# Optimization experiments

Measured on AMD Instinct MI355X. Metric: run time of the kernel, lower is better.

## Reference

```python
import jax, jax.numpy as jnp
import numpy as np
import math

C = 512
NUM_HEADS = 4
GROUPS = 32  # group_count(512, 32)
EPS = 1e-5


def group_norm(x, gamma, beta):
    # x: [b, c, h, w]; normalize over (c//GROUPS, h, w) per group
    b, c, h, w = x.shape
    xg = x.reshape(b, GROUPS, -1)
    mu = jnp.mean(xg, axis=-1, keepdims=True)
    var = jnp.var(xg, axis=-1, keepdims=True)
    xn = ((xg - mu) * jax.lax.rsqrt(var + EPS)).reshape(b, c, h, w)
    return xn * gamma[None, :, None, None] + beta[None, :, None, None]


def setup_inputs() -> dict:
    key = jax.random.key(0)
    ks = jax.random.split(key, 5)
    b, h, w = 2, 64, 64
    x = jax.random.normal(ks[0], (b, C, h, w), dtype=jnp.float32)
    gn_w = jnp.ones((C,), dtype=jnp.float32)
    gn_b = jnp.zeros((C,), dtype=jnp.float32)
    s_qkv = 1.0 / math.sqrt(C)
    w_qkv = jax.random.uniform(ks[1], (3 * C, C), jnp.float32, -s_qkv, s_qkv)
    b_qkv = jax.random.uniform(ks[2], (3 * C,), jnp.float32, -s_qkv, s_qkv)
    w_proj = jax.random.uniform(ks[3], (C, C), jnp.float32, -s_qkv, s_qkv)
    b_proj = jax.random.uniform(ks[4], (C,), jnp.float32, -s_qkv, s_qkv)
    return {"x": x, "gn_w": gn_w, "gn_b": gn_b, "w_qkv": w_qkv,
            "b_qkv": b_qkv, "w_proj": w_proj, "b_proj": b_proj}


def reference(x, gn_w, gn_b, w_qkv, b_qkv, w_proj, b_proj):
    b, c, h, w = x.shape
    L = h * w
    nh = NUM_HEADS
    hd = c // nh
    residual = x
    xn = group_norm(x, gn_w, gn_b).reshape(b, c, L)
    # Conv1d with kernel_size=1 == channelwise linear: [b, 3c, L]
    qkv = jnp.einsum('bcl,oc->bol', xn, w_qkv) + b_qkv[None, :, None]
    q, k, v = jnp.split(qkv, 3, axis=1)
    q = q.reshape(b, nh, hd, L)
    k = k.reshape(b, nh, hd, L)
    v = v.reshape(b, nh, hd, L)
    scores = jnp.einsum('bncd,bnce->bnde', q, k) / math.sqrt(hd)
    attn = jax.nn.softmax(scores, axis=-1)
    out = jnp.einsum('bnde,bnce->bncd', attn, v).reshape(b, c, L)
    out = jnp.einsum('bcl,oc->bol', out, w_proj) + b_proj[None, :, None]
    return out.reshape(b, c, h, w) + residual
```

## Files before the change

### kernel.cpp

```cpp
#include <hip/hip_runtime.h>
#include <math.h>

typedef __bf16 bf16;
typedef __bf16 bf16x8 __attribute__((ext_vector_type(8)));
typedef __bf16 bf16x4 __attribute__((ext_vector_type(4)));
typedef float f32x4 __attribute__((ext_vector_type(4)));

#define QSCALE (0.08838834764831845f * 1.4426950408889634f)

__device__ __forceinline__ void gll16(const bf16* g, bf16* l) {
    __builtin_amdgcn_global_load_lds((const __attribute__((address_space(1))) void*)g,
                                     (__attribute__((address_space(3))) void*)l, 16, 0, 0);
}

__global__ void k_pre(const float* __restrict__ wqkv, const float* __restrict__ wproj,
                      const float* __restrict__ x,
                      bf16* __restrict__ wqkv_b, bf16* __restrict__ wproj_b,
                      float* __restrict__ part) {
    int blk = blockIdx.x;
    if (blk < 1024) {
        int i = blk * 256 + threadIdx.x;
        const int n1 = (1536 * 512) / 4;
        float4 v;
        bf16* dst;
        if (i < n1) { v = ((const float4*)wqkv)[i];      dst = wqkv_b + (size_t)i * 4; }
        else        { v = ((const float4*)wproj)[i - n1]; dst = wproj_b + (size_t)(i - n1) * 4; }
        bf16x4 o;
        o[0] = (bf16)v.x; o[1] = (bf16)v.y; o[2] = (bf16)v.z; o[3] = (bf16)v.w;
        *(bf16x4*)dst = o;
        return;
    }
    int b2 = blk - 1024;
    int grp = b2 >> 2, p = b2 & 3;
    const float4* src = (const float4*)(x + (size_t)grp * 65536 + (size_t)p * 16384);
    float s = 0.f, ss = 0.f;
    for (int it = 0; it < 16; ++it) {
        float4 v = src[threadIdx.x + it * 256];
        s  += v.x + v.y + v.z + v.w;
        ss += v.x * v.x + v.y * v.y + v.z * v.z + v.w * v.w;
    }
    for (int off = 32; off; off >>= 1) { s += __shfl_down(s, off); ss += __shfl_down(ss, off); }
    __shared__ float rs[4], rss[4];
    int wave = threadIdx.x >> 6;
    if ((threadIdx.x & 63) == 0) { rs[wave] = s; rss[wave] = ss; }
    __syncthreads();
    if (threadIdx.x == 0) {
        part[(grp * 4 + p) * 2]     = rs[0] + rs[1] + rs[2] + rs[3];
        part[(grp * 4 + p) * 2 + 1] = rss[0] + rss[1] + rss[2] + rss[3];
    }
}

__global__ __launch_bounds__(256) void k_gn_norm_t(const float* __restrict__ x, const float* __restrict__ gw,
                                                   const float* __restrict__ gb, const float* __restrict__ part,
                                                   bf16* __restrict__ xn_t) {
    __shared__ float sX[64 * 69];
    __shared__ float sMean[4], sRstd[4];
    int b = blockIdx.z, c0 = blockIdx.y * 64, l0 = blockIdx.x * 64;
    int t = threadIdx.x;
    if (t < 4) {
        int g = b * 32 + (c0 >> 4) + t;
        float S = 0.f, SS = 0.f;
        for (int p = 0; p < 4; ++p) { S += part[(g * 4 + p) * 2]; SS += part[(g * 4 + p) * 2 + 1]; }
        float mean = S * (1.f / 65536.f);
        float var  = SS * (1.f / 65536.f) - mean * mean;
        sMean[t] = mean;
        sRstd[t] = rsqrtf(var + 1e-5f);
    }
    __syncthreads();
    int cr = t >> 4, lq = t & 15;
    const float* xp = x + ((size_t)(b * 512 + c0)) * 4096 + l0;
    for (int i = 0; i < 4; ++i) {
        int c = cr + i * 16;
        int cg = c0 + c;
        float mean = sMean[c >> 4], rstd = sRstd[c >> 4];
        float ga = gw[cg] * rstd;
        float be = gb[cg] - mean * ga;
        float4 v = *(const float4*)(xp + (size_t)c * 4096 + lq * 4);
        float* d = &sX[c * 69 + lq * 4];
        d[0] = v.x * ga + be; d[1] = v.y * ga + be; d[2] = v.z * ga + be; d[3] = v.w * ga + be;
    }
    __syncthreads();
    int lr = t >> 3, cp = t & 7;
    bf16* dst = xn_t + ((size_t)b * 4096 + l0) * 512 + c0;
    for (int i = 0; i < 2; ++i) {
        int l = lr + i * 32;
        bf16x8 o;
        for (int j = 0; j < 8; ++j) o[j] = (bf16)sX[(cp * 8 + j) * 69 + l];
        *(bf16x8*)(dst + (size_t)l * 512 + cp * 8) = o;
    }
}

__global__ __launch_bounds__(256, 3) void k_gemm_qkv(
    const bf16* __restrict__ A, const bf16* __restrict__ W, const float* __restrict__ bias,
    bf16* __restrict__ qkT, bf16* __restrict__ vb) {
    constexpr int BUF = (128 + 128) * 32;
    __shared__ bf16 smem[17408];
    int bz = blockIdx.z;
    int m0 = blockIdx.y * 128, n0 = blockIdx.x * 128;
    int tid = threadIdx.x, lane = tid & 63, wave = tid >> 6;
    int lo = lane & 15, quad = lane >> 4;
    int mw = (wave >> 1) * 64, nw = (wave & 1) * 64;
    int srcswz = (((lane & 3) ^ ((lane >> 2) & 3) ^ ((lane >> 4) & 3)) * 8);
    const bf16* aptr[2]; int adst[2];
    const bf16* bptr[2]; int bdst[2];
    for (int i = 0; i < 2; ++i) {
        int r0 = wave * 32 + i * 16;
        int row = r0 + (lane >> 2);
        aptr[i] = A + (size_t)bz * (4096 * 512) + (size_t)(m0 + row) * 512 + srcswz;
        adst[i] = r0 * 32;
        bptr[i] = W + (size_t)(n0 + row) * 512 + srcswz;
        bdst[i] = 128 * 32 + r0 * 32;
    }
    f32x4 acc[4][4] = {};
    for (int i = 0; i < 2; ++i) {
        gll16(aptr[i], &smem[adst[i]]); aptr[i] += 32;
        gll16(bptr[i], &smem[bdst[i]]); bptr[i] += 32;
    }
    int sw = (quad ^ (lo & 3) ^ (lo >> 2)) * 8;
    for (int step = 0; step < 16; ++step) {
        int cur = step & 1;
        __syncthreads();
        if (step < 15) {
            bf16* nb = &smem[(cur ^ 1) * BUF];
            for (int i = 0; i < 2; ++i) {
                gll16(aptr[i], nb + adst[i]); aptr[i] += 32;
                gll16(bptr[i], nb + bdst[i]); bptr[i] += 32;
            }
        }
        const bf16* sA = &smem[cur * BUF];
        const bf16* sB = sA + 128 * 32;
        bf16x8 af[4], bfr[4];
        for (int t = 0; t < 4; ++t) af[t]  = *(const bf16x8*)&sA[(mw + t * 16 + lo) * 32 + sw];
        for (int t = 0; t < 4; ++t) bfr[t] = *(const bf16x8*)&sB[(nw + t * 16 + lo) * 32 + sw];
        for (int mt = 0; mt < 4; ++mt)
            for (int nt = 0; nt < 4; ++nt)
                acc[mt][nt] = __builtin_amdgcn_mfma_f32_16x16x32_bf16(af[mt], bfr[nt], acc[mt][nt], 0, 0, 0);
    }
    __syncthreads();
    bf16* sT = smem;
    bool isv = (n0 >= 1024);
    float sc = (n0 < 512) ? QSCALE : 1.f;
    for (int mt = 0; mt < 4; ++mt)
        for (int nt = 0; nt < 4; ++nt) {
            int c = nw + nt * 16 + lo;
            float bv = bias[n0 + c];
            for (int r = 0; r < 4; ++r) {
                int l = mw + mt * 16 + quad * 4 + r;
                float v = (acc[mt][nt][r] + bv) * sc;
                if (isv) sT[c * 136 + l] = (bf16)v;
                else     sT[l * 136 + c] = (bf16)v;
            }
        }
    __syncthreads();
    int row = tid >> 1, hh = tid & 1;
    if (isv) {
        bf16* dst = vb + (size_t)bz * (512 * 4096) + (size_t)(n0 - 1024 + row) * 4096 + m0;
        for (int j = 0; j < 8; ++j) {
            int ch = hh + j * 2;
            *(bf16x8*)(dst + ch * 8) = *(const bf16x8*)&sT[row * 136 + ch * 8];
        }
    } else {
        bf16* dst = qkT + (size_t)bz * (4096 * 1024) + (size_t)(m0 + row) * 1024 + n0;
        for (int j = 0; j < 8; ++j) {
            int ch = hh + j * 2;
            *(bf16x8*)(dst + ch * 8) = *(const bf16x8*)&sT[row * 136 + ch * 8];
        }
    }
}

__global__ __launch_bounds__(256, 3) void k_gemm_proj(
    const bf16* __restrict__ W, const bf16* __restrict__ Bm,
    const float* __restrict__ bias_m,
    float* __restrict__ outf, const float* __restrict__ resid) {
    constexpr int BUF = (64 + 128) * 64;
    __shared__ bf16 smem[2 * BUF];
    int bz = blockIdx.z;
    int m0 = blockIdx.y * 64, n0 = blockIdx.x * 128;
    int tid = threadIdx.x, lane = tid & 63, wave = tid >> 6;
    int lo = lane & 15, quad = lane >> 4;
    int lr = lane >> 3, ls = lane & 7;
    int mw = (wave >> 1) * 32, nw = (wave & 1) * 64;
    const bf16* aptr[2]; int adst[2];
    for (int i = 0; i < 2; ++i) {
        int r0 = wave * 16 + i * 8;
        int row = r0 + lr;
        aptr[i] = W + (size_t)(m0 + row) * 512 + ((ls ^ (row & 7)) * 8);
        adst[i] = r0 * 64;
    }
    const bf16* bptr[4]; int bdst[4];
    for (int i = 0; i < 4; ++i) {
        int r0 = wave * 32 + i * 8;
        int row = r0 + lr;
        bptr[i] = Bm + (size_t)bz * (4096 * 512) + (size_t)(n0 + row) * 512 + ((ls ^ (row & 7)) * 8);
        bdst[i] = 64 * 64 + r0 * 64;
    }
    f32x4 acc[2][4] = {};
    for (int i = 0; i < 2; ++i) { gll16(aptr[i], &smem[adst[i]]); aptr[i] += 64; }
    for (int i = 0; i < 4; ++i) { gll16(bptr[i], &smem[bdst[i]]); bptr[i] += 64; }
    for (int step = 0; step < 8; ++step) {
        int cur = step & 1;
        __syncthreads();
        if (step < 7) {
            bf16* nb = &smem[(cur ^ 1) * BUF];
            for (int i = 0; i < 2; ++i) { gll16(aptr[i], nb + adst[i]); aptr[i] += 64; }
            for (int i = 0; i < 4; ++i) { gll16(bptr[i], nb + bdst[i]); bptr[i] += 64; }
        }
        const bf16* sA = &smem[cur * BUF];
        const bf16* sB = sA + 64 * 64;
        for (int kk = 0; kk < 2; ++kk) {
            bf16x8 af[2], bfr[4];
            int sw = ((kk * 4 + quad) ^ (lo & 7)) * 8;
            for (int t = 0; t < 2; ++t) af[t]  = *(const bf16x8*)&sA[(mw + t * 16 + lo) * 64 + sw];
            for (int t = 0; t < 4; ++t) bfr[t] = *(const bf16x8*)&sB[(nw + t * 16 + lo) * 64 + sw];
            for (int mt = 0; mt < 2; ++mt)
                for (int nt = 0; nt < 4; ++nt)
                    acc[mt][nt] = __builtin_amdgcn_mfma_f32_16x16x32_bf16(af[mt], bfr[nt], acc[mt][nt], 0, 0, 0);
        }
    }
    for (int mt = 0; mt < 2; ++mt) {
        int rowb = m0 + mw + mt * 16 + quad * 4;
        for (int nt = 0; nt < 4; ++nt) {
            int col = n0 + nw + nt * 16 + lo;
            for (int r = 0; r < 4; ++r) {
                int row = rowb + r;
                size_t idx = (size_t)bz * (512 * 4096) + (size_t)row * 4096 + col;
                outf[idx] = acc[mt][nt][r] + bias_m[row] + resid[idx];
            }
        }
    }
}

__global__ __launch_bounds__(512, 2) void k_attn(const bf16* __restrict__ qkT, const bf16* __restrict__ vmat,
                                                 bf16* __restrict__ attnT) {
    __shared__ __align__(16) char smem[104448];
    bf16* sE = (bf16*)smem;
    float* sStat = (float*)(smem + 102400);
    int bidx = blockIdx.x;
    int bh = bidx & 7;
    int bb = bh >> 2, h = bh & 3;
    int l0 = (bidx >> 3) * 128;
    int tid = threadIdx.x, lane = tid & 63, wave = tid >> 6;
    int lo = lane & 15, quad = lane >> 4;
    int a = wave & 3, b2 = wave >> 2;
    int lr16 = lane >> 4, ls16 = lane & 15;
    int lr8 = lane >> 3, ls8 = lane & 7;
    const bf16* qbase = qkT + ((size_t)bb * 4096 + l0) * 1024 + h * 128;
    const bf16* kbase = qkT + (size_t)bb * 4096 * 1024 + 512 + h * 128;
    const bf16* vbase = vmat + (size_t)(bb * 512 + h * 128) * 4096;
    for (int i = 0; i < 4; ++i) {
        int r0 = wave * 16 + i * 4;
        int row = r0 + lr16;
        gll16(qbase + (size_t)row * 1024 + ((ls16 ^ (row & 15)) * 8), sE + r0 * 128);
    }
    __syncthreads();
    bf16x8 qf[2][4];
    for (int nt = 0; nt < 2; ++nt) {
        int row = a * 32 + nt * 16 + lo;
        for (int kk = 0; kk < 4; ++kk)
            qf[nt][kk] = *(const bf16x8*)&sE[row * 128 + (((kk * 4 + quad) ^ lo) * 8)];
    }
    __syncthreads();
    const bf16* kptr[2]; int kdst[2];
    const bf16* vptr[2]; int vdst[2];
    for (int i = 0; i < 2; ++i) {
        int r0 = wave * 8 + i * 4;
        int row = r0 + lr16;
        kptr[i] = kbase + (size_t)row * 1024 + ((ls16 ^ (row & 15)) * 8);
        kdst[i] = r0 * 128;
        int s0 = wave * 16 + i * 8;
        int srow = s0 + lr8;
        vptr[i] = vbase + (size_t)srow * 4096 + ((ls8 ^ (srow & 7)) * 8);
        vdst[i] = s0 * 64;
    }
    bf16* sPe = (bf16*)(smem + 65536) + wave * 1280;
    float l_r[2];
    l_r[0] = l_r[1] = 0.f;
    f32x4 oacc[8][2] = {};
    for (int i = 0; i < 2; ++i) { gll16(kptr[i], sE + kdst[i]); kptr[i] += (size_t)64 * 1024; }
    for (int i = 0; i < 2; ++i) { gll16(vptr[i], sE + 16384 + vdst[i]); vptr[i] += 64; }
    for (int it = 0; it < 64; ++it) {
        int cur = it & 1;
        __syncthreads();
        if (it < 63) {
            bf16* nk = sE + (cur ^ 1) * 8192;
            bf16* nv = sE + 16384 + (cur ^ 1) * 8192;
            for (int i = 0; i < 2; ++i) { gll16(kptr[i], nk + kdst[i]); kptr[i] += (size_t)64 * 1024; }
            for (int i = 0; i < 2; ++i) { gll16(vptr[i], nv + vdst[i]); vptr[i] += 64; }
        }
        const bf16* sK = sE + cur * 8192;
        const bf16* sV = sE + 16384 + cur * 8192;
        f32x4 s[2][2];
        for (int mt = 0; mt < 2; ++mt) {
            int krow = b2 * 32 + mt * 16 + lo;
            bf16x8 kf[4];
            for (int kk = 0; kk < 4; ++kk)
                kf[kk] = *(const bf16x8*)&sK[krow * 128 + (((kk * 4 + quad) ^ lo) * 8)];
            for (int nt = 0; nt < 2; ++nt) {
                f32x4 acc = {};
                for (int kk = 0; kk < 4; ++kk)
                    acc = __builtin_amdgcn_mfma_f32_16x16x32_bf16(kf[kk], qf[nt][kk], acc, 0, 0, 0);
                s[mt][nt] = acc;
            }
        }
        for (int nt = 0; nt < 2; ++nt) {
            float sm = 0.f;
            for (int mt = 0; mt < 2; ++mt) {
                bf16x4 pk;
                for (int r = 0; r < 4; ++r) {
                    float pv = __builtin_amdgcn_exp2f(s[mt][nt][r]);
                    sm += pv;
                    pk[r] = (bf16)pv;
                }
                *(bf16x4*)&sPe[(nt * 16 + lo) * 40 + mt * 16 + quad * 4] = pk;
            }
            l_r[nt] += sm;
        }
        bf16x8 pf[2];
        for (int nt = 0; nt < 2; ++nt)
            pf[nt] = *(const bf16x8*)&sPe[(nt * 16 + lo) * 40 + quad * 8];
        for (int mt2 = 0; mt2 < 8; ++mt2) {
            bf16x8 vf = *(const bf16x8*)&sV[(mt2 * 16 + lo) * 64 + (((b2 * 4 + quad) ^ (lo & 7)) * 8)];
            for (int nt = 0; nt < 2; ++nt)
                oacc[mt2][nt] = __builtin_amdgcn_mfma_f32_16x16x32_bf16(vf, pf[nt], oacc[mt2][nt], 0, 0, 0);
        }
    }
    for (int nt = 0; nt < 2; ++nt) {
        l_r[nt] += __shfl_xor(l_r[nt], 16);
        l_r[nt] += __shfl_xor(l_r[nt], 32);
    }
    __syncthreads();
    if (quad == 0) {
        for (int nt = 0; nt < 2; ++nt) {
            int qb = a * 32 + nt * 16 + lo;
            sStat[qb * 2 + b2] = l_r[nt];
        }
    }
    __syncthreads();
    float inv[2];
    for (int nt = 0; nt < 2; ++nt) {
        int qb = a * 32 + nt * 16 + lo;
        inv[nt] = 1.f / (sStat[qb * 2] + sStat[qb * 2 + 1]);
    }
    float* sOm = (float*)smem;
    bf16* sOut = (bf16*)(smem + 67584);
    if (b2 == 1) {
        for (int mt2 = 0; mt2 < 8; ++mt2)
            for (int nt = 0; nt < 2; ++nt)
                for (int r = 0; r < 4; ++r) {
                    int vc = mt2 * 16 + quad * 4 + r;
                    sOm[a * 4224 + vc * 33 + nt * 16 + lo] = oacc[mt2][nt][r];
                }
    }
    __syncthreads();
    if (b2 == 0) {
        for (int mt2 = 0; mt2 < 8; ++mt2)
            for (int nt = 0; nt < 2; ++nt)
                for (int r = 0; r < 4; ++r) {
                    int vc = mt2 * 16 + quad * 4 + r;
                    float v = (oacc[mt2][nt][r] + sOm[a * 4224 + vc * 33 + nt * 16 + lo]) * inv[nt];
                    sOut[(a * 32 + nt * 16 + lo) * 136 + vc] = (bf16)v;
                }
    }
    __syncthreads();
    bf16* dst = attnT + ((size_t)bb * 4096 + l0) * 512 + h * 128;
    for (int i = 0; i < 4; ++i) {
        int row = (tid >> 4) + i * 32;
        int chunk = tid & 15;
        bf16x8 v = *(const bf16x8*)&sOut[row * 136 + chunk * 8];
        *(bf16x8*)(dst + (size_t)row * 512 + chunk * 8) = v;
    }
}

extern "C" void kernel_launch(void* const* d_in, const int* in_sizes, int n_in,
                              void* d_out, int out_size, void* d_ws, size_t ws_size,
                              hipStream_t stream) {
    const float* x      = (const float*)d_in[0];
    const float* gn_w   = (const float*)d_in[1];
    const float* gn_b   = (const float*)d_in[2];
    const float* w_qkv  = (const float*)d_in[3];
    const float* b_qkv  = (const float*)d_in[4];
    const float* w_proj = (const float*)d_in[5];
    const float* b_proj = (const float*)d_in[6];
    float* out = (float*)d_out;
    char* ws = (char*)d_ws;
    bf16* wqkv_b  = (bf16*)(ws + 0);
    bf16* wproj_b = (bf16*)(ws + 1572864);
    bf16* xn_t    = (bf16*)(ws + 2097152);
    bf16* qkT     = (bf16*)(ws + 10485760);
    bf16* vb      = (bf16*)(ws + 27262976);
    bf16* attnT   = (bf16*)(ws + 35651584);
    float* part   = (float*)(ws + 44040192);

    k_pre<<<1280, 256, 0, stream>>>(w_qkv, w_proj, x, wqkv_b, wproj_b, part);
    k_gn_norm_t<<<dim3(64, 8, 2), 256, 0, stream>>>(x, gn_w, gn_b, part, xn_t);
    k_gemm_qkv<<<dim3(12, 32, 2), 256, 0, stream>>>(xn_t, wqkv_b, b_qkv, qkT, vb);
    k_attn<<<256, 512, 0, stream>>>(qkT, vb, attnT);
    k_gemm_proj<<<dim3(32, 8, 2), 256, 0, stream>>>(wproj_b, attnT, b_proj, out, x);
}
```

Before: 192.1 us.

## Single-buffer QKV GEMM with BK=64, XOR swizzle and block remapping

The QKV GEMM mainloop drops double-buffered BK=32 staging in favour of single-buffered BK=64 tiles. This halves the number of barrier-separated steps but removes the overlap between loads and MFMA. The LDS swizzle becomes an 8-way XOR over 64-element rows to avoid bank conflicts. Block indices are remapped so that consecutive workgroups spread across the tile space, aiming at better L2 locality across XCDs.

```diff
diff --git a/kernel.cpp b/kernel.cpp
--- a/kernel.cpp
+++ b/kernel.cpp
@@ -93,48 +93,45 @@
 __global__ __launch_bounds__(256, 3) void k_gemm_qkv(
     const bf16* __restrict__ A, const bf16* __restrict__ W, const float* __restrict__ bias,
     bf16* __restrict__ qkT, bf16* __restrict__ vb) {
-    constexpr int BUF = (128 + 128) * 32;
     __shared__ bf16 smem[17408];
-    int bz = blockIdx.z;
-    int m0 = blockIdx.y * 128, n0 = blockIdx.x * 128;
+    int linear = blockIdx.x + 12 * blockIdx.y + 384 * blockIdx.z;
+    int swz = (linear & 7) * 96 + (linear >> 3);
+    int n0 = (swz % 12) * 128;
+    int m0 = ((swz / 12) % 32) * 128;
+    int bz = swz / 384;
     int tid = threadIdx.x, lane = tid & 63, wave = tid >> 6;
     int lo = lane & 15, quad = lane >> 4;
+    int lr = lane >> 3, ls = lane & 7;
     int mw = (wave >> 1) * 64, nw = (wave & 1) * 64;
-    int srcswz = (((lane & 3) ^ ((lane >> 2) & 3) ^ ((lane >> 4) & 3)) * 8);
-    const bf16* aptr[2]; int adst[2];
-    const bf16* bptr[2]; int bdst[2];
-    for (int i = 0; i < 2; ++i) {
-        int r0 = wave * 32 + i * 16;
-        int row = r0 + (lane >> 2);
-        aptr[i] = A + (size_t)bz * (4096 * 512) + (size_t)(m0 + row) * 512 + srcswz;
-        adst[i] = r0 * 32;
-        bptr[i] = W + (size_t)(n0 + row) * 512 + srcswz;
-        bdst[i] = 128 * 32 + r0 * 32;
+    const bf16* aptr[4]; int adst[4];
+    const bf16* bptr[4]; int bdst[4];
+    for (int i = 0; i < 4; ++i) {
+        int r0 = wave * 32 + i * 8;
+        int row = r0 + lr;
+        aptr[i] = A + (size_t)bz * (4096 * 512) + (size_t)(m0 + row) * 512 + ((ls ^ (row & 7)) * 8);
+        adst[i] = r0 * 64;
+        bptr[i] = W + (size_t)(n0 + row) * 512 + ((ls ^ (row & 7)) * 8);
+        bdst[i] = 8192 + r0 * 64;
     }
     f32x4 acc[4][4] = {};
-    for (int i = 0; i < 2; ++i) {
-        gll16(aptr[i], &smem[adst[i]]); aptr[i] += 32;
-        gll16(bptr[i], &smem[bdst[i]]); bptr[i] += 32;
-    }
-    int sw = (quad ^ (lo & 3) ^ (lo >> 2)) * 8;
-    for (int step = 0; step < 16; ++step) {
-        int cur = step & 1;
+    for (int step = 0; step < 8; ++step) {
         __syncthreads();
-        if (step < 15) {
-            bf16* nb = &smem[(cur ^ 1) * BUF];
-            for (int i = 0; i < 2; ++i) {
-                gll16(aptr[i], nb + adst[i]); aptr[i] += 32;
-                gll16(bptr[i], nb + bdst[i]); bptr[i] += 32;
-            }
-        }
-        const bf16* sA = &smem[cur * BUF];
-        const bf16* sB = sA + 128 * 32;
-        bf16x8 af[4], bfr[4];
-        for (int t = 0; t < 4; ++t) af[t]  = *(const bf16x8*)&sA[(mw + t * 16 + lo) * 32 + sw];
-        for (int t = 0; t < 4; ++t) bfr[t] = *(const bf16x8*)&sB[(nw + t * 16 + lo) * 32 + sw];
-        for (int mt = 0; mt < 4; ++mt)
-            for (int nt = 0; nt < 4; ++nt)
-                acc[mt][nt] = __builtin_amdgcn_mfma_f32_16x16x32_bf16(af[mt], bfr[nt], acc[mt][nt], 0, 0, 0);
+        for (int i = 0; i < 4; ++i) {
+            gll16(aptr[i], &smem[adst[i]]); aptr[i] += 64;
+            gll16(bptr[i], &smem[bdst[i]]); bptr[i] += 64;
+        }
+        __syncthreads();
+        const bf16* sA = smem;
+        const bf16* sB = smem + 8192;
+        for (int kk = 0; kk < 2; ++kk) {
+            bf16x8 af[4], bfr[4];
+            int sw = ((kk * 4 + quad) ^ (lo & 7)) * 8;
+            for (int t = 0; t < 4; ++t) af[t]  = *(const bf16x8*)&sA[(mw + t * 16 + lo) * 64 + sw];
+            for (int t = 0; t < 4; ++t) bfr[t] = *(const bf16x8*)&sB[(nw + t * 16 + lo) * 64 + sw];
+            for (int mt = 0; mt < 4; ++mt)
+                for (int nt = 0; nt < 4; ++nt)
+                    acc[mt][nt] = __builtin_amdgcn_mfma_f32_16x16x32_bf16(af[mt], bfr[nt], acc[mt][nt], 0, 0, 0);
+        }
     }
     __syncthreads();
     bf16* sT = smem;
```

New measurement: 186.8 us. 1.03x faster.
